# Performance work log

Hardware: AMD Instinct MI355X
Metric: run time of the kernel (lower is better)

The kernel has to match this reference:

```python
import jax, jax.numpy as jnp
import numpy as np

N = 50000
E = 800000
FEAT, ACT = 96, 32
HID, HEADS = 64, 4
NEG_SLOPE = 0.2


def gat_conv(x, src, dst, W, att_s, att_d, bias):
    # x: [N, F_in]; W: [F_in, H*C]; att_s/att_d: [H, C]; bias: [H*C]
    H, C = att_s.shape
    h = (x @ W).reshape(-1, H, C)                      # [N, H, C]
    a_s = jnp.einsum('nhc,hc->nh', h, att_s)           # [N, H]
    a_d = jnp.einsum('nhc,hc->nh', h, att_d)
    e = jax.nn.leaky_relu(a_s[src] + a_d[dst], NEG_SLOPE)  # [E, H]
    m = jax.ops.segment_max(e, dst, num_segments=N)
    e = jnp.exp(e - m[dst])
    denom = jax.ops.segment_sum(e, dst, num_segments=N)
    alpha = e / (denom[dst] + 1e-16)                   # softmax over incoming edges
    out = jax.ops.segment_sum(alpha[:, :, None] * h[src], dst, num_segments=N)
    return out.reshape(-1, H * C) + bias


def setup_inputs() -> dict:
    key = jax.random.key(0)
    ks = jax.random.split(key, 12)
    node_features = jax.random.normal(ks[0], (N, FEAT), dtype=jnp.float32)
    actions = jax.random.normal(ks[1], (N, ACT), dtype=jnp.float32)
    edge_index = jax.random.randint(ks[2], (2, E), 0, N, dtype=jnp.int64)
    s = 0.1
    return {
        'node_features': node_features,
        'actions': actions,
        'edge_index': edge_index,
        'W_emb': jax.random.normal(ks[3], (FEAT + ACT, HID), dtype=jnp.float32) * s,
        'b_emb': jnp.zeros((HID,), dtype=jnp.float32),
        'W1': jax.random.normal(ks[4], (HID, HEADS * HID), dtype=jnp.float32) * s,
        'att_s1': jax.random.normal(ks[5], (HEADS, HID), dtype=jnp.float32) * s,
        'att_d1': jax.random.normal(ks[6], (HEADS, HID), dtype=jnp.float32) * s,
        'b1': jnp.zeros((HEADS * HID,), dtype=jnp.float32),
        'W2': jax.random.normal(ks[7], (HEADS * HID, HID), dtype=jnp.float32) * s,
        'att_s2': jax.random.normal(ks[8], (1, HID), dtype=jnp.float32) * s,
        'att_d2': jax.random.normal(ks[9], (1, HID), dtype=jnp.float32) * s,
        'b2': jnp.zeros((HID,), dtype=jnp.float32),
        'W_v': jax.random.normal(ks[10], (HID, 1), dtype=jnp.float32) * s,
        'b_v': jnp.zeros((1,), dtype=jnp.float32),
    }


def reference(node_features, actions, edge_index, W_emb, b_emb, W1, att_s1, att_d1, b1,
              W2, att_s2, att_d2, b2, W_v, b_v):
    # add self loops (PyG GATConv default add_self_loops=True)
    loop = jnp.arange(N, dtype=edge_index.dtype)
    src = jnp.concatenate([edge_index[0], loop])
    dst = jnp.concatenate([edge_index[1], loop])
    x = jnp.concatenate([node_features, actions], axis=1)
    x = x @ W_emb + b_emb
    x = jax.nn.relu(gat_conv(x, src, dst, W1, att_s1, att_d1, b1))
    x = jax.nn.relu(gat_conv(x, src, dst, W2, att_s2, att_d2, b2))
    g = jnp.mean(x, axis=0, keepdims=True)  # [1, HID]
    return g @ W_v + b_v                    # [1, 1]
```

## Files before the change

### kernel.cpp

```cpp
#include <hip/hip_runtime.h>
#include <hip/hip_bf16.h>
#include <math.h>

#define FEAT 96
#define ACTF 32

using frag8 = __attribute__((ext_vector_type(8))) short;
using f32x4 = __attribute__((ext_vector_type(4))) float;

__device__ __forceinline__ float lrelu(float x) { return x >= 0.f ? x : 0.2f * x; }
__device__ __forceinline__ void atomAddF(float* p, float v) {
    __hip_atomic_fetch_add(p, v, __ATOMIC_RELAXED, __HIP_MEMORY_SCOPE_AGENT);
}
__device__ __forceinline__ float expc(float x) { return __expf(fminf(x, 60.f)); }
__device__ __forceinline__ unsigned short f2bf(float f) {
    __hip_bfloat16 h = __float2bfloat16(f);
    return *(unsigned short*)&h;
}
__device__ __forceinline__ float bf2f(unsigned short u) {
    return __uint_as_float((unsigned)u << 16);
}

__global__ __launch_bounds__(256) void xprep(
    const float* __restrict__ nf, const float* __restrict__ act,
    unsigned short* __restrict__ Xh, unsigned short* __restrict__ Xl, long long total) {
    long long i = (long long)blockIdx.x * 256 + threadIdx.x;
    if (i >= total) return;
    int n = (int)(i >> 7), k = (int)(i & 127);
    float v = (k < FEAT) ? nf[(size_t)n * FEAT + k] : act[(size_t)n * ACTF + (k - FEAT)];
    unsigned short h = f2bf(v);
    Xh[i] = h;
    Xl[i] = f2bf(v - bf2f(h));
}

__global__ void w1prep(const float* __restrict__ Wemb, const float* __restrict__ bemb,
                       const float* __restrict__ W1,
                       unsigned short* __restrict__ wfh, unsigned short* __restrict__ wfl,
                       float* __restrict__ bfused) {
    int k = blockIdx.x, c = threadIdx.x;
    if (k < 128) {
        float s = 0.f;
        for (int j = 0; j < 64; ++j) s = fmaf(Wemb[k * 64 + j], W1[j * 256 + c], s);
        unsigned short h = f2bf(s);
        wfh[(size_t)c * 128 + k] = h;
        wfl[(size_t)c * 128 + k] = f2bf(s - bf2f(h));
    } else {
        float s = 0.f;
        for (int j = 0; j < 64; ++j) s = fmaf(bemb[j], W1[j * 256 + c], s);
        bfused[c] = s;
    }
}

__global__ __launch_bounds__(256, 2) void gemm1_mfma_w(
    const unsigned short* __restrict__ Xh, const unsigned short* __restrict__ Xl,
    const unsigned short* __restrict__ wfh, const unsigned short* __restrict__ wfl,
    const float* __restrict__ bfused, const float* __restrict__ att_s,
    const float* __restrict__ att_d, __hip_bfloat16* __restrict__ h1b,
    float* __restrict__ a_s, float* __restrict__ a_d, int N) {
    int w = threadIdx.x >> 6, l = threadIdx.x & 63;
    int r16 = l & 15, kg = l >> 4;
    frag8 bh[4][4], bl[4][4];
    #pragma unroll
    for (int c = 0; c < 4; ++c) {
        int ct = w * 4 + c;
        const short* bhp = (const short*)wfh + (size_t)(ct * 16 + r16) * 128 + kg * 8;
        const short* blp = (const short*)wfl + (size_t)(ct * 16 + r16) * 128 + kg * 8;
        #pragma unroll
        for (int ks = 0; ks < 4; ++ks) {
            bh[c][ks] = *(const frag8*)(bhp + ks * 32);
            bl[c][ks] = *(const frag8*)(blp + ks * 32);
        }
    }
    float biasv[4], awv[4], dwv[4];
    #pragma unroll
    for (int c = 0; c < 4; ++c) {
        int ch = w * 64 + c * 16 + r16;
        biasv[c] = bfused[ch];
        awv[c] = att_s[ch];
        dwv[c] = att_d[ch];
    }
    int ntiles = (N + 15) >> 4;
    for (int tile = blockIdx.x; tile < ntiles; tile += gridDim.x) {
        int nb = tile * 16;
        int arow = nb + r16; if (arow >= N) arow = N - 1;
        const short* ahp = (const short*)Xh + (size_t)arow * 128 + kg * 8;
        const short* alp = (const short*)Xl + (size_t)arow * 128 + kg * 8;
        frag8 ah[4], al[4];
        #pragma unroll
        for (int ks = 0; ks < 4; ++ks) {
            ah[ks] = *(const frag8*)(ahp + ks * 32);
            al[ks] = *(const frag8*)(alp + ks * 32);
        }
        float s_s[4] = {0.f, 0.f, 0.f, 0.f}, s_d[4] = {0.f, 0.f, 0.f, 0.f};
        #pragma unroll
        for (int c = 0; c < 4; ++c) {
            f32x4 acc = (f32x4){0.f, 0.f, 0.f, 0.f};
            #pragma unroll
            for (int ks = 0; ks < 4; ++ks) {
                acc = __builtin_amdgcn_mfma_f32_16x16x32_bf16(ah[ks], bh[c][ks], acc, 0, 0, 0);
                acc = __builtin_amdgcn_mfma_f32_16x16x32_bf16(al[ks], bh[c][ks], acc, 0, 0, 0);
                acc = __builtin_amdgcn_mfma_f32_16x16x32_bf16(ah[ks], bl[c][ks], acc, 0, 0, 0);
            }
            int ch = w * 64 + c * 16 + r16;
            #pragma unroll
            for (int r = 0; r < 4; ++r) {
                int node = nb + kg * 4 + r;
                float v = acc[r] + biasv[c];
                if (node < N) h1b[(size_t)node * 256 + ch] = __float2bfloat16(v);
                s_s[r] = fmaf(v, awv[c], s_s[r]);
                s_d[r] = fmaf(v, dwv[c], s_d[r]);
            }
        }
        #pragma unroll
        for (int r = 0; r < 4; ++r) {
            float vs = s_s[r], vd = s_d[r];
            #pragma unroll
            for (int o = 1; o < 16; o <<= 1) {
                vs += __shfl_xor(vs, o);
                vd += __shfl_xor(vd, o);
            }
            int node = nb + kg * 4 + r;
            if (r16 == 0 && node < N) {
                a_s[(size_t)node * 4 + w] = vs;
                a_d[(size_t)node * 4 + w] = vd;
            }
        }
    }
}

__global__ void w2_prep(const float* __restrict__ W2, __hip_bfloat16* __restrict__ w2t) {
    int i = blockIdx.x * 256 + threadIdx.x;
    int k = i >> 6, c = i & 63;
    w2t[(size_t)c * 256 + k] = __float2bfloat16(W2[i]);
}

__global__ __launch_bounds__(256) void gemm2_mfma(
    const __hip_bfloat16* __restrict__ out1b, const __hip_bfloat16* __restrict__ w2t,
    const float* __restrict__ att_s, const float* __restrict__ att_d,
    __hip_bfloat16* __restrict__ h2b, float* __restrict__ a_s, float* __restrict__ a_d,
    int N) {
    int w = threadIdx.x >> 6, l = threadIdx.x & 63;
    int nb = (blockIdx.x * 4 + w) * 16;
    if (nb >= N) return;
    int r16 = l & 15, kg = l >> 4;
    const short* A = (const short*)out1b;
    int arow = min(nb + r16, N - 1);
    const short* arp = A + (size_t)arow * 256 + kg * 8;
    frag8 a[8];
    #pragma unroll
    for (int ks = 0; ks < 8; ++ks) a[ks] = *(const frag8*)(arp + ks * 32);
    const short* B = (const short*)w2t;
    f32x4 acc[4];
    #pragma unroll
    for (int ct = 0; ct < 4; ++ct) {
        acc[ct] = (f32x4){0.f, 0.f, 0.f, 0.f};
        const short* brp = B + (size_t)(ct * 16 + r16) * 256 + kg * 8;
        #pragma unroll
        for (int ks = 0; ks < 8; ++ks) {
            frag8 b = *(const frag8*)(brp + ks * 32);
            acc[ct] = __builtin_amdgcn_mfma_f32_16x16x32_bf16(a[ks], b, acc[ct], 0, 0, 0);
        }
    }
    float s_s[4] = {0.f, 0.f, 0.f, 0.f}, s_d[4] = {0.f, 0.f, 0.f, 0.f};
    #pragma unroll
    for (int ct = 0; ct < 4; ++ct) {
        int ch = ct * 16 + r16;
        float aw = att_s[ch], dw = att_d[ch];
        #pragma unroll
        for (int r = 0; r < 4; ++r) {
            int node = nb + kg * 4 + r;
            float v = acc[ct][r];
            if (node < N) h2b[(size_t)node * 64 + ch] = __float2bfloat16(v);
            s_s[r] = fmaf(v, aw, s_s[r]);
            s_d[r] = fmaf(v, dw, s_d[r]);
        }
    }
    #pragma unroll
    for (int r = 0; r < 4; ++r) {
        #pragma unroll
        for (int o = 1; o < 16; o <<= 1) {
            s_s[r] += __shfl_xor(s_s[r], o);
            s_d[r] += __shfl_xor(s_d[r], o);
        }
        int node = nb + kg * 4 + r;
        if (r16 == 0 && node < N) { a_s[node] = s_s[r]; a_d[node] = s_d[r]; }
    }
}

__global__ void hist_kernel(const int* __restrict__ dst, int* __restrict__ cnt, int E, int ET) {
    int e = blockIdx.x * blockDim.x + threadIdx.x;
    if (e >= ET) return;
    int d = (e < E) ? dst[e] : (e - E);
    atomicAdd(&cnt[d], 1);
}

__global__ __launch_bounds__(256) void scan_blocks(
    const int* __restrict__ cnt, int* __restrict__ off, int* __restrict__ bsum, int n) {
    int b = blockIdx.x, t = threadIdx.x;
    int i = b * 256 + t;
    int v = (i < n) ? cnt[i] : 0;
    int lane = t & 63, w = t >> 6;
    int x = v;
    #pragma unroll
    for (int o = 1; o < 64; o <<= 1) {
        int y = __shfl_up(x, o);
        if (lane >= o) x += y;
    }
    __shared__ int wtot[4];
    if (lane == 63) wtot[w] = x;
    __syncthreads();
    int add = 0;
    #pragma unroll
    for (int j = 0; j < 4; ++j) if (j < w) add += wtot[j];
    int incl = x + add;
    if (i < n) off[i] = incl - v;
    if (t == 255) bsum[b] = incl;
}

__global__ __launch_bounds__(256) void scan_tops(
    const int* __restrict__ bsum, int* __restrict__ bpre, int nb) {
    int t = threadIdx.x;
    int v = (t < nb) ? bsum[t] : 0;
    int lane = t & 63, w = t >> 6;
    int x = v;
    #pragma unroll
    for (int o = 1; o < 64; o <<= 1) {
        int y = __shfl_up(x, o);
        if (lane >= o) x += y;
    }
    __shared__ int wtot[4];
    if (lane == 63) wtot[w] = x;
    __syncthreads();
    int add = 0;
    #pragma unroll
    for (int j = 0; j < 4; ++j) if (j < w) add += wtot[j];
    if (t < nb) bpre[t] = x + add - v;
    if (t == 255) bpre[nb] = x + add;
}

__global__ __launch_bounds__(256) void scan_add(
    const int* __restrict__ bpre, int* __restrict__ off, int n, int nb) {
    int b = blockIdx.x, t = threadIdx.x;
    int i = b * 256 + t;
    if (i < n) off[i] += bpre[b];
    if (b == 0 && t == 0) off[n] = bpre[nb];
}

__global__ void scatter_kernel(const int* __restrict__ src, const int* __restrict__ dst,
                               const int* __restrict__ off, int* __restrict__ cur,
                               int* __restrict__ perm, int E, int ET) {
    int e = blockIdx.x * blockDim.x + threadIdx.x;
    if (e >= ET) return;
    int s = (e < E) ? src[e] : (e - E);
    int d = (e < E) ? dst[e] : (e - E);
    int r = atomicAdd(&cur[d], 1);
    perm[off[d] + r] = s;
}

__global__ __launch_bounds__(256) void fused_gat4(
    const int* __restrict__ off, const int* __restrict__ perm,
    const float* __restrict__ a_s, const float* __restrict__ a_d,
    const __hip_bfloat16* __restrict__ h1b, const float* __restrict__ bias,
    __hip_bfloat16* __restrict__ out1b, int N) {
    __shared__ float exls[4][64][4];
    __shared__ unsigned idxls[4][64];
    int w = threadIdx.x >> 6, l = threadIdx.x & 63;
    int d = blockIdx.x * 4 + w;
    if (d >= N) return;
    int lo = off[d], hi = off[d + 1];
    const float4* as4 = (const float4*)a_s;
    float4 ad = ((const float4*)a_d)[d];
    float dx = 0.f, dy = 0.f, dz = 0.f, dw = 0.f;
    for (int e = lo + l; e < hi; e += 64) {
        float4 a = as4[perm[e]];
        dx += expc(lrelu(a.x + ad.x));
        dy += expc(lrelu(a.y + ad.y));
        dz += expc(lrelu(a.z + ad.z));
        dw += expc(lrelu(a.w + ad.w));
    }
    #pragma unroll
    for (int o = 32; o; o >>= 1) {
        dx += __shfl_xor(dx, o); dy += __shfl_xor(dy, o);
        dz += __shfl_xor(dz, o); dw += __shfl_xor(dw, o);
    }
    int g = l >> 4;
    float rr = 1.f / ((g == 0 ? dx : g == 1 ? dy : g == 2 ? dz : dw) + 1e-16f);
    const char* hb = (const char*)h1b;
    unsigned laneoff = (unsigned)l * 8u;
    float acc0 = 0.f, acc1 = 0.f, acc2 = 0.f, acc3 = 0.f;
    for (int base = lo; base < hi; base += 64) {
        int e = base + l;
        if (e < hi) {
            int s = perm[e];
            float4 a = as4[s];
            exls[w][l][0] = expc(lrelu(a.x + ad.x));
            exls[w][l][1] = expc(lrelu(a.y + ad.y));
            exls[w][l][2] = expc(lrelu(a.z + ad.z));
            exls[w][l][3] = expc(lrelu(a.w + ad.w));
            idxls[w][l] = (unsigned)s * 512u;
        }
        int n = min(64, hi - base);
        #pragma unroll 4
        for (int i = 0; i < n; ++i) {
            float ex = exls[w][i][g];
            unsigned voff = idxls[w][i] + laneoff;
            uint2 v = *(const uint2*)(hb + voff);
            float f0 = __uint_as_float(v.x << 16);
            float f1 = __uint_as_float(v.x & 0xffff0000u);
            float f2 = __uint_as_float(v.y << 16);
            float f3 = __uint_as_float(v.y & 0xffff0000u);
            acc0 = fmaf(ex, f0, acc0);
            acc1 = fmaf(ex, f1, acc1);
            acc2 = fmaf(ex, f2, acc2);
            acc3 = fmaf(ex, f3, acc3);
        }
    }
    float4 bv = ((const float4*)bias)[l];
    ushort4 o4;
    o4.x = f2bf(fmaxf(fmaf(acc0, rr, bv.x), 0.f));
    o4.y = f2bf(fmaxf(fmaf(acc1, rr, bv.y), 0.f));
    o4.z = f2bf(fmaxf(fmaf(acc2, rr, bv.z), 0.f));
    o4.w = f2bf(fmaxf(fmaf(acc3, rr, bv.w), 0.f));
    ((ushort4*)out1b)[(size_t)d * 64 + l] = o4;
}

__global__ __launch_bounds__(256) void fused_gat1(
    const int* __restrict__ off, const int* __restrict__ perm,
    const float* __restrict__ a_s, const float* __restrict__ a_d,
    const __hip_bfloat16* __restrict__ h2b, const float* __restrict__ bias,
    float* __restrict__ out2, int N) {
    __shared__ float2 alds[4][64];
    int w = threadIdx.x >> 6, l = threadIdx.x & 63;
    int d = blockIdx.x * 4 + w;
    if (d >= N) return;
    int lo = off[d], hi = off[d + 1];
    float add = a_d[d];
    float den = 0.f;
    for (int e = lo + l; e < hi; e += 64)
        den += expc(lrelu(a_s[perm[e]] + add));
    #pragma unroll
    for (int o = 32; o; o >>= 1) den += __shfl_xor(den, o);
    float rr = 1.f / (den + 1e-16f);
    const char* hb = (const char*)h2b;
    unsigned laneoff = (unsigned)l * 2u;
    float acc = 0.f;
    for (int base = lo; base < hi; base += 64) {
        int e = base + l;
        if (e < hi) {
            int s = perm[e];
            float ex = expc(lrelu(a_s[s] + add));
            alds[w][l] = make_float2(ex, __uint_as_float((unsigned)s * 128u));
        }
        int n = min(64, hi - base);
        #pragma unroll 4
        for (int i = 0; i < n; ++i) {
            float2 p = alds[w][i];
            unsigned voff = __float_as_uint(p.y) + laneoff;
            unsigned u = *(const unsigned short*)(hb + voff);
            acc = fmaf(p.x, __uint_as_float(u << 16), acc);
        }
    }
    out2[(size_t)d * 64 + l] = fmaxf(fmaf(acc, rr, bias[l]), 0.f);
}

__global__ void colsum_kernel(const float* __restrict__ x, float* __restrict__ g, int N) {
    __shared__ float part[4][64];
    int c = threadIdx.x & 63;
    int r = threadIdx.x >> 6;
    float acc = 0.f;
    for (long long n = (long long)blockIdx.x * 4 + r; n < N; n += (long long)gridDim.x * 4)
        acc += x[n * 64 + c];
    part[r][c] = acc;
    __syncthreads();
    if (r == 0) {
        float v = part[0][c] + part[1][c] + part[2][c] + part[3][c];
        atomAddF(&g[c], v);
    }
}

__global__ void final_kernel(const float* __restrict__ g, const float* __restrict__ Wv,
                             const float* __restrict__ bv, float* __restrict__ out, int N) {
    int lane = threadIdx.x;
    float v = (g[lane] / (float)N) * Wv[lane];
    #pragma unroll
    for (int off = 32; off; off >>= 1) v += __shfl_down(v, off);
    if (lane == 0) out[0] = v + bv[0];
}

extern "C" void kernel_launch(void* const* d_in, const int* in_sizes, int n_in,
                              void* d_out, int out_size, void* d_ws, size_t ws_size,
                              hipStream_t stream) {
    const float* nf   = (const float*)d_in[0];
    const float* act  = (const float*)d_in[1];
    const int*   ei   = (const int*)d_in[2];
    const float* Wemb = (const float*)d_in[3];
    const float* bemb = (const float*)d_in[4];
    const float* W1   = (const float*)d_in[5];
    const float* as1  = (const float*)d_in[6];
    const float* ad1  = (const float*)d_in[7];
    const float* b1   = (const float*)d_in[8];
    const float* W2   = (const float*)d_in[9];
    const float* as2  = (const float*)d_in[10];
    const float* ad2  = (const float*)d_in[11];
    const float* b2   = (const float*)d_in[12];
    const float* Wv   = (const float*)d_in[13];
    const float* bv   = (const float*)d_in[14];
    float* out = (float*)d_out;

    const int N = in_sizes[0] / FEAT;
    const int E = in_sizes[2] / 2;
    const int ET = E + N;
    const int* srcp = ei;
    const int* dstp = ei + E;
    const int NB = (N + 255) / 256;

    char* ws = (char*)d_ws;
    unsigned short* Xh = (unsigned short*)ws;
    unsigned short* Xl = Xh + (size_t)N * 128;
    __hip_bfloat16* h1b   = (__hip_bfloat16*)(Xl + (size_t)N * 128);
    __hip_bfloat16* out1b = h1b + (size_t)N * 256;
    float* a_s  = (float*)(out1b + (size_t)N * 256);
    float* a_d  = a_s + (size_t)N * 4;
    __hip_bfloat16* h2b = (__hip_bfloat16*)(a_d + (size_t)N * 4);
    float* out2 = (float*)(h2b + (size_t)N * 64);
    float* g    = out2 + (size_t)N * 64;
    __hip_bfloat16* w2t = (__hip_bfloat16*)(g + 64);
    unsigned short* wfh = (unsigned short*)(w2t + 64 * 256);
    unsigned short* wfl = wfh + 256 * 128;
    float* bfused = (float*)(wfl + 256 * 128);
    int* cnt  = (int*)Xh;
    int* off  = cnt + N;
    int* cur  = off + N + 1;
    int* perm = cur + N;
    int* bsum = perm + ET;
    int* bpre = bsum + NB;

    (void)ws_size; (void)n_in; (void)out_size;

    long long xtot = (long long)N * 128;
    xprep<<<(int)((xtot + 255) / 256), 256, 0, stream>>>(nf, act, Xh, Xl, xtot);
    w1prep<<<129, 256, 0, stream>>>(Wemb, bemb, W1, wfh, wfl, bfused);
    w2_prep<<<64, 256, 0, stream>>>(W2, w2t);

    gemm1_mfma_w<<<1024, 256, 0, stream>>>(Xh, Xl, wfh, wfl, bfused,
                                           as1, ad1, h1b, a_s, a_d, N);

    hipMemsetAsync(cnt, 0, (size_t)N * sizeof(int), stream);
    hipMemsetAsync(cur, 0, (size_t)N * sizeof(int), stream);
    hist_kernel<<<(ET + 255) / 256, 256, 0, stream>>>(dstp, cnt, E, ET);
    scan_blocks<<<NB, 256, 0, stream>>>(cnt, off, bsum, N);
    scan_tops<<<1, 256, 0, stream>>>(bsum, bpre, NB);
    scan_add<<<NB, 256, 0, stream>>>(bpre, off, N, NB);
    scatter_kernel<<<(ET + 255) / 256, 256, 0, stream>>>(srcp, dstp, off, cur, perm, E, ET);

    fused_gat4<<<(N + 3) / 4, 256, 0, stream>>>(off, perm, a_s, a_d, h1b, b1, out1b, N);

    gemm2_mfma<<<(N + 63) / 64, 256, 0, stream>>>(out1b, w2t, as2, ad2, h2b, a_s, a_d, N);
    fused_gat1<<<(N + 3) / 4, 256, 0, stream>>>(off, perm, a_s, a_d, h2b, b2, out2, N);

    hipMemsetAsync(g, 0, 64 * sizeof(float), stream);
    colsum_kernel<<<512, 256, 0, stream>>>(out2, g, N);
    final_kernel<<<1, 64, 0, stream>>>(g, Wv, bv, out, N);
}
```

Measured before the change: 293.8 us.

## Widen per-lane gathers in GAT aggregation and split edges across half-waves

```diff
diff --git a/kernel.cpp b/kernel.cpp
--- a/kernel.cpp
+++ b/kernel.cpp
@@ -20,6 +20,8 @@
 __device__ __forceinline__ float bf2f(unsigned short u) {
     return __uint_as_float((unsigned)u << 16);
 }
+__device__ __forceinline__ float bflo(unsigned u) { return __uint_as_float(u << 16); }
+__device__ __forceinline__ float bfhi(unsigned u) { return __uint_as_float(u & 0xffff0000u); }
 
 __global__ __launch_bounds__(256) void xprep(
     const float* __restrict__ nf, const float* __restrict__ act,
@@ -283,45 +285,56 @@
         dx += __shfl_xor(dx, o); dy += __shfl_xor(dy, o);
         dz += __shfl_xor(dz, o); dw += __shfl_xor(dw, o);
     }
-    int g = l >> 4;
-    float rr = 1.f / ((g == 0 ? dx : g == 1 ? dy : g == 2 ? dz : dw) + 1e-16f);
+    int eg = l >> 5;
+    int li = l & 31;
+    int gh = li >> 3;
+    float rr = 1.f / ((gh == 0 ? dx : gh == 1 ? dy : gh == 2 ? dz : dw) + 1e-16f);
     const char* hb = (const char*)h1b;
-    unsigned laneoff = (unsigned)l * 8u;
-    float acc0 = 0.f, acc1 = 0.f, acc2 = 0.f, acc3 = 0.f;
+    unsigned laneoff = (unsigned)li * 16u;
+    float acc[8] = {0.f, 0.f, 0.f, 0.f, 0.f, 0.f, 0.f, 0.f};
     for (int base = lo; base < hi; base += 64) {
         int e = base + l;
-        if (e < hi) {
-            int s = perm[e];
-            float4 a = as4[s];
-            exls[w][l][0] = expc(lrelu(a.x + ad.x));
-            exls[w][l][1] = expc(lrelu(a.y + ad.y));
-            exls[w][l][2] = expc(lrelu(a.z + ad.z));
-            exls[w][l][3] = expc(lrelu(a.w + ad.w));
-            idxls[w][l] = (unsigned)s * 512u;
-        }
+        bool valid = e < hi;
+        int s = valid ? perm[e] : 0;
+        float4 a = as4[s];
+        exls[w][l][0] = valid ? expc(lrelu(a.x + ad.x)) : 0.f;
+        exls[w][l][1] = valid ? expc(lrelu(a.y + ad.y)) : 0.f;
+        exls[w][l][2] = valid ? expc(lrelu(a.z + ad.z)) : 0.f;
+        exls[w][l][3] = valid ? expc(lrelu(a.w + ad.w)) : 0.f;
+        idxls[w][l] = valid ? (unsigned)s * 512u : 0u;
         int n = min(64, hi - base);
-        #pragma unroll 4
-        for (int i = 0; i < n; ++i) {
-            float ex = exls[w][i][g];
-            unsigned voff = idxls[w][i] + laneoff;
-            uint2 v = *(const uint2*)(hb + voff);
-            float f0 = __uint_as_float(v.x << 16);
-            float f1 = __uint_as_float(v.x & 0xffff0000u);
-            float f2 = __uint_as_float(v.y << 16);
-            float f3 = __uint_as_float(v.y & 0xffff0000u);
-            acc0 = fmaf(ex, f0, acc0);
-            acc1 = fmaf(ex, f1, acc1);
-            acc2 = fmaf(ex, f2, acc2);
-            acc3 = fmaf(ex, f3, acc3);
-        }
-    }
-    float4 bv = ((const float4*)bias)[l];
-    ushort4 o4;
-    o4.x = f2bf(fmaxf(fmaf(acc0, rr, bv.x), 0.f));
-    o4.y = f2bf(fmaxf(fmaf(acc1, rr, bv.y), 0.f));
-    o4.z = f2bf(fmaxf(fmaf(acc2, rr, bv.z), 0.f));
-    o4.w = f2bf(fmaxf(fmaf(acc3, rr, bv.w), 0.f));
-    ((ushort4*)out1b)[(size_t)d * 64 + l] = o4;
+        #pragma unroll 2
+        for (int i = 0; i < n; i += 2) {
+            int ii = i + eg;
+            float ex = exls[w][ii][gh];
+            unsigned voff = idxls[w][ii] + laneoff;
+            uint4 v = *(const uint4*)(hb + voff);
+            acc[0] = fmaf(ex, bflo(v.x), acc[0]);
+            acc[1] = fmaf(ex, bfhi(v.x), acc[1]);
+            acc[2] = fmaf(ex, bflo(v.y), acc[2]);
+            acc[3] = fmaf(ex, bfhi(v.y), acc[3]);
+            acc[4] = fmaf(ex, bflo(v.z), acc[4]);
+            acc[5] = fmaf(ex, bfhi(v.z), acc[5]);
+            acc[6] = fmaf(ex, bflo(v.w), acc[6]);
+            acc[7] = fmaf(ex, bfhi(v.w), acc[7]);
+        }
+    }
+    #pragma unroll
+    for (int j = 0; j < 8; ++j) acc[j] += __shfl_xor(acc[j], 32);
+    if (eg == 0) {
+        float4 b0 = ((const float4*)bias)[li * 2];
+        float4 b1 = ((const float4*)bias)[li * 2 + 1];
+        uint4 pk;
+        pk.x = (unsigned)f2bf(fmaxf(fmaf(acc[0], rr, b0.x), 0.f))
+             | ((unsigned)f2bf(fmaxf(fmaf(acc[1], rr, b0.y), 0.f)) << 16);
+        pk.y = (unsigned)f2bf(fmaxf(fmaf(acc[2], rr, b0.z), 0.f))
+             | ((unsigned)f2bf(fmaxf(fmaf(acc[3], rr, b0.w), 0.f)) << 16);
+        pk.z = (unsigned)f2bf(fmaxf(fmaf(acc[4], rr, b1.x), 0.f))
+             | ((unsigned)f2bf(fmaxf(fmaf(acc[5], rr, b1.y), 0.f)) << 16);
+        pk.w = (unsigned)f2bf(fmaxf(fmaf(acc[6], rr, b1.z), 0.f))
+             | ((unsigned)f2bf(fmaxf(fmaf(acc[7], rr, b1.w), 0.f)) << 16);
+        ((uint4*)(out1b + (size_t)d * 256))[li] = pk;
+    }
 }
 
 __global__ __launch_bounds__(256) void fused_gat1(
@@ -329,7 +342,8 @@
     const float* __restrict__ a_s, const float* __restrict__ a_d,
     const __hip_bfloat16* __restrict__ h2b, const float* __restrict__ bias,
     float* __restrict__ out2, int N) {
-    __shared__ float2 alds[4][64];
+    __shared__ float exls1[4][64];
+    __shared__ unsigned idxls1[4][64];
     int w = threadIdx.x >> 6, l = threadIdx.x & 63;
     int d = blockIdx.x * 4 + w;
     if (d >= N) return;
@@ -341,26 +355,47 @@
     #pragma unroll
     for (int o = 32; o; o >>= 1) den += __shfl_xor(den, o);
     float rr = 1.f / (den + 1e-16f);
+    int eg = l >> 4;
+    int li = l & 15;
     const char* hb = (const char*)h2b;
-    unsigned laneoff = (unsigned)l * 2u;
-    float acc = 0.f;
+    unsigned laneoff = (unsigned)li * 8u;
+    float acc0 = 0.f, acc1 = 0.f, acc2 = 0.f, acc3 = 0.f;
     for (int base = lo; base < hi; base += 64) {
         int e = base + l;
-        if (e < hi) {
-            int s = perm[e];
-            float ex = expc(lrelu(a_s[s] + add));
-            alds[w][l] = make_float2(ex, __uint_as_float((unsigned)s * 128u));
-        }
+        bool valid = e < hi;
+        int s = valid ? perm[e] : 0;
+        exls1[w][l] = valid ? expc(lrelu(a_s[s] + add)) : 0.f;
+        idxls1[w][l] = valid ? (unsigned)s * 128u : 0u;
         int n = min(64, hi - base);
         #pragma unroll 4
-        for (int i = 0; i < n; ++i) {
-            float2 p = alds[w][i];
-            unsigned voff = __float_as_uint(p.y) + laneoff;
-            unsigned u = *(const unsigned short*)(hb + voff);
-            acc = fmaf(p.x, __uint_as_float(u << 16), acc);
-        }
-    }
-    out2[(size_t)d * 64 + l] = fmaxf(fmaf(acc, rr, bias[l]), 0.f);
+        for (int i = 0; i < n; i += 4) {
+            int ii = i + eg;
+            float ex = exls1[w][ii];
+            unsigned voff = idxls1[w][ii] + laneoff;
+            uint2 v = *(const uint2*)(hb + voff);
+            acc0 = fmaf(ex, bflo(v.x), acc0);
+            acc1 = fmaf(ex, bfhi(v.x), acc1);
+            acc2 = fmaf(ex, bflo(v.y), acc2);
+            acc3 = fmaf(ex, bfhi(v.y), acc3);
+        }
+    }
+    #pragma unroll
+    for (int o = 16; o < 64; o <<= 1) {
+        acc0 += __shfl_xor(acc0, o);
+        acc1 += __shfl_xor(acc1, o);
+        acc2 += __shfl_xor(acc2, o);
+        acc3 += __shfl_xor(acc3, o);
+    }
+    if (eg == 0 && (l >> 4) == 0) {
+        const float4* b4 = (const float4*)bias;
+        float4 bv = b4[li];
+        float4 o4;
+        o4.x = fmaxf(fmaf(acc0, rr, bv.x), 0.f);
+        o4.y = fmaxf(fmaf(acc1, rr, bv.y), 0.f);
+        o4.z = fmaxf(fmaf(acc2, rr, bv.z), 0.f);
+        o4.w = fmaxf(fmaf(acc3, rr, bv.w), 0.f);
+        ((float4*)(out2 + (size_t)d * 64))[li] = o4;
+    }
 }
 
 __global__ void colsum_kernel(const float* __restrict__ x, float* __restrict__ g, int N) {
```

New measurement: 297.6 us. About the same (+1.3%).
